# Optimization experiments

Measured on AMD Instinct MI355X. Metric: run time of the kernel, lower is better.

Reference implementation:

```python
import jax, jax.numpy as jnp
import numpy as np

B, T, D = 4, 2048, 1024

def setup_inputs() -> dict:
    key = jax.random.key(0)
    kx, kq, kk, kv = jax.random.split(key, 4)
    lim = 1.0 / np.sqrt(D)
    x = jax.random.normal(kx, (B, T, D), dtype=jnp.float32)
    # nn.Linear weights (stored as [out,in]); applied as x @ W.T
    W_q = jax.random.uniform(kq, (D, D), jnp.float32, -lim, lim)
    W_k = jax.random.uniform(kk, (D, D), jnp.float32, -lim, lim)
    W_v = jax.random.uniform(kv, (D, D), jnp.float32, -lim, lim)
    return {"x": x, "W_q": W_q, "W_k": W_k, "W_v": W_v}

def reference(x, W_q, W_k, W_v):
    d = x.shape[-1]
    Q = jnp.einsum('btd,ed->bte', x, W_q)
    K = jnp.einsum('btd,ed->bte', x, W_k)
    V = jnp.einsum('btd,ed->bte', x, W_v)
    att = jnp.einsum('bqd,bkd->bqk', Q, K) / jnp.sqrt(jnp.asarray(d, x.dtype))
    weights = jax.nn.softmax(att, axis=-1)  # NOTE: original applies no causal mask
    return jnp.einsum('bqk,bkd->bqd', weights, V)
```

## Files before the change

kernel.cpp:

```cpp
#include <hip/hip_runtime.h>
#include <hip/hip_bf16.h>
#include <math.h>
#include <type_traits>


typedef short shortx8 __attribute__((ext_vector_type(8)));
typedef short shortx4 __attribute__((ext_vector_type(4)));
typedef float floatx16 __attribute__((ext_vector_type(16)));
typedef __attribute__((address_space(3))) void lds_void_t;
typedef __attribute__((address_space(1))) const void gmem_void_t;

#define GLD16(gp, lp) \
    __builtin_amdgcn_global_load_lds((gmem_void_t*)(gp), (lds_void_t*)(lp), 16, 0, 0)

#define MODE_PROJ 0
#define MODE_EXP  1
#define MODE_DIV  2

template <int MODE>
__global__ __launch_bounds__(512, 4) void mfma_gemm_abt(
    const __hip_bfloat16* __restrict__ A, const __hip_bfloat16* __restrict__ B,
    void* __restrict__ Cv, float* __restrict__ rowsum,
    __hip_bfloat16* __restrict__ Vt,
    int M, int N, int K, long sA, long sB, long sC, float alpha)
{
    __shared__ __hip_bfloat16 lds[2 * 12288];

    using CT = std::conditional_t<MODE == MODE_DIV, float, __hip_bfloat16>;

    const int z = blockIdx.z;
    A += (long)z * sA;
    B += (long)z * sB;
    CT* C = (CT*)Cv + (long)z * sC;

    const int t     = threadIdx.x;
    const int wave  = t >> 6;
    const int lane  = t & 63;
    const int m0    = blockIdx.x * 256;
    const int n0    = blockIdx.y * 128;
    const int wm    = (wave >> 1) * 64;
    const int wn    = (wave & 1) * 64;
    const int lrow  = lane & 31;
    const int lhalf = lane >> 5;

    const long KU   = (long)(K >> 4);
    const long aOff = (long)((m0 >> 5) + wave) * KU * 512 + lane * 8;
    const long bOff = ((long)((n0 >> 5) + (wave >> 1)) * KU + (wave & 1)) * 512
                      + lane * 8;
    const int  dA   = wave * 1024;
    const int  dB   = 8192 + wave * 512;

    const int raB = (wave >> 1) * 2048 + lane * 8;
    const int rbB = 8192 + (wave & 1) * 2048 + lane * 8;

#define STAGE(bo_, k2_) do {                                               \
        GLD16(A + aOff + (long)(k2_) * 512,       lds + (bo_) + dA);       \
        GLD16(A + aOff + (long)((k2_) + 1) * 512, lds + (bo_) + dA + 512); \
        GLD16(B + bOff + (long)(k2_) * 512,       lds + (bo_) + dB);       \
    } while (0)

    floatx16 acc[2][2] = {};
    const int KT = K >> 5;

    STAGE(0, 0);
    asm volatile("s_waitcnt vmcnt(0)" ::: "memory");
    __builtin_amdgcn_s_barrier();

    for (int kt = 0; kt < KT; ++kt) {
        if (kt + 1 < KT)
            STAGE(((kt + 1) & 1) * 12288, 2 * (kt + 1));

        const __hip_bfloat16* Ls = lds + (kt & 1) * 12288;

        #pragma unroll
        for (int s = 0; s < 2; ++s) {
            shortx8 a[2], b[2];
            #pragma unroll
            for (int i = 0; i < 2; ++i)
                a[i] = *(const shortx8*)(Ls + raB + (2 * i + s) * 512);
            #pragma unroll
            for (int j = 0; j < 2; ++j)
                b[j] = *(const shortx8*)(Ls + rbB + (2 * j + s) * 512);
            __builtin_amdgcn_s_setprio(1);
            #pragma unroll
            for (int i = 0; i < 2; ++i)
                #pragma unroll
                for (int j = 0; j < 2; ++j)
                    acc[i][j] = __builtin_amdgcn_mfma_f32_32x32x16_bf16(
                        a[i], b[j], acc[i][j], 0, 0, 0);
            __builtin_amdgcn_s_setprio(0);
        }
        asm volatile("s_waitcnt vmcnt(0)" ::: "memory");
        __builtin_amdgcn_s_barrier();
    }
#undef STAGE

    auto sidx = [&](int row, int col) -> long {
        return ((long)(row >> 5) * (N >> 4) + (col >> 4)) * 512
             + ((row & 31) + 32 * ((col >> 3) & 1)) * 8 + (col & 7);
    };

    if constexpr (MODE == MODE_PROJ) {
        if (z == 2) {
            const int bz   = m0 >> 11;
            const long bo  = (long)bz * N * 2048;
            #pragma unroll
            for (int i = 0; i < 2; ++i)
                #pragma unroll
                for (int j = 0; j < 2; ++j)
                    #pragma unroll
                    for (int g = 0; g < 4; ++g) {
                        const int t0 = (m0 + wm + 32 * i + g * 8 + 4 * lhalf) & 2047;
                        const int d  = n0 + wn + 32 * j + lrow;
                        shortx4 pk;
                        #pragma unroll
                        for (int r = 0; r < 4; ++r) {
                            __hip_bfloat16 hb = __float2bfloat16(acc[i][j][4 * g + r]);
                            pk[r] = *(short*)&hb;
                        }
                        const long idx = bo
                            + ((long)(d >> 5) * 128 + (t0 >> 4)) * 512
                            + ((d & 31) + 32 * ((t0 >> 3) & 1)) * 8 + (t0 & 7);
                        *(shortx4*)(Vt + idx) = pk;
                    }
        } else {
            #pragma unroll
            for (int i = 0; i < 2; ++i)
                #pragma unroll
                for (int j = 0; j < 2; ++j)
                    #pragma unroll
                    for (int g = 0; g < 4; ++g)
                        #pragma unroll
                        for (int r = 0; r < 4; ++r) {
                            const int row = m0 + wm + 32 * i + g * 8 + 4 * lhalf + r;
                            const int col = n0 + wn + 32 * j + lrow;
                            C[sidx(row, col)] = __float2bfloat16(acc[i][j][4 * g + r]);
                        }
        }
    } else if constexpr (MODE == MODE_EXP) {
        #pragma unroll
        for (int i = 0; i < 2; ++i) {
            float rs[16];
            #pragma unroll
            for (int reg = 0; reg < 16; ++reg) rs[reg] = 0.0f;
            #pragma unroll
            for (int j = 0; j < 2; ++j)
                #pragma unroll
                for (int g = 0; g < 4; ++g)
                    #pragma unroll
                    for (int r = 0; r < 4; ++r) {
                        const int row = m0 + wm + 32 * i + g * 8 + 4 * lhalf + r;
                        const int col = n0 + wn + 32 * j + lrow;
                        const float e = __expf(acc[i][j][4 * g + r] * alpha);
                        rs[4 * g + r] += e;
                        C[sidx(row, col)] = __float2bfloat16(e);
                    }
            #pragma unroll
            for (int reg = 0; reg < 16; ++reg) {
                float v = rs[reg];
                v += __shfl_xor(v, 1);
                v += __shfl_xor(v, 2);
                v += __shfl_xor(v, 4);
                v += __shfl_xor(v, 8);
                v += __shfl_xor(v, 16);
                if (lrow == 0) {
                    const long row = m0 + wm + 32 * i + (reg >> 2) * 8 + 4 * lhalf + (reg & 3);
                    atomicAdd(&rowsum[(long)z * M + row], v);
                }
            }
        }
    } else {
        #pragma unroll
        for (int i = 0; i < 2; ++i) {
            float inv[16];
            #pragma unroll
            for (int g = 0; g < 4; ++g)
                #pragma unroll
                for (int r = 0; r < 4; ++r) {
                    const long row = m0 + wm + 32 * i + g * 8 + 4 * lhalf + r;
                    inv[4 * g + r] = 1.0f / rowsum[(long)z * M + row];
                }
            #pragma unroll
            for (int j = 0; j < 2; ++j)
                #pragma unroll
                for (int g = 0; g < 4; ++g)
                    #pragma unroll
                    for (int r = 0; r < 4; ++r) {
                        const long row = m0 + wm + 32 * i + g * 8 + 4 * lhalf + r;
                        const long col = n0 + wn + 32 * j + lrow;
                        C[row * N + col] = acc[i][j][4 * g + r] * inv[4 * g + r];
                    }
        }
    }
}

__global__ __launch_bounds__(256) void prep(
    const float* __restrict__ x,
    const float* __restrict__ W0, const float* __restrict__ W1,
    const float* __restrict__ W2,
    __hip_bfloat16* __restrict__ xb, __hip_bfloat16* __restrict__ Wb,
    float* __restrict__ rowsum, int n4x, int n4w)
{
    const long i = (long)blockIdx.x * 256 + threadIdx.x;
    if (i < 2048) {
        float4 zz; zz.x = zz.y = zz.z = zz.w = 0.0f;
        ((float4*)rowsum)[i] = zz;
    }
    const float* src;
    __hip_bfloat16* dst;
    long j;
    if (i < n4x) {
        src = x; dst = xb; j = i;
    } else {
        const long k = i - n4x;
        const int w  = (int)(k >> 18);
        j = k & (n4w - 1);
        src = (w == 0) ? W0 : (w == 1) ? W1 : W2;
        dst = Wb + (long)w * n4w * 4;
    }
    const float4 f = ((const float4*)src)[j];
    const int row = (int)(j >> 8);
    const int k0  = (int)(j & 255) * 4;
    const long idx = ((long)(row >> 5) * 64 + (k0 >> 4)) * 512
                   + ((row & 31) + 32 * ((k0 >> 3) & 1)) * 8 + (k0 & 7);
    shortx4 pk;
    __hip_bfloat16 h0 = __float2bfloat16(f.x); pk[0] = *(short*)&h0;
    __hip_bfloat16 h1 = __float2bfloat16(f.y); pk[1] = *(short*)&h1;
    __hip_bfloat16 h2 = __float2bfloat16(f.z); pk[2] = *(short*)&h2;
    __hip_bfloat16 h3 = __float2bfloat16(f.w); pk[3] = *(short*)&h3;
    *(shortx4*)(dst + idx) = pk;
}

extern "C" void kernel_launch(void* const* d_in, const int* in_sizes, int n_in,
                              void* d_out, int out_size, void* d_ws, size_t ws_size,
                              hipStream_t stream)
{
    constexpr int  Bb = 4, T = 2048, D = 1024;
    constexpr int  M  = Bb * T;
    constexpr long TD = (long)T * D;
    constexpr long TT = (long)T * T;
    constexpr long MD = (long)M * D;

    const float* x  = (const float*)d_in[0];
    const float* Wq = (const float*)d_in[1];
    const float* Wk = (const float*)d_in[2];
    const float* Wv = (const float*)d_in[3];
    float* out = (float*)d_out;

    __hip_bfloat16* Q  = (__hip_bfloat16*)d_ws;
    __hip_bfloat16* Kb = Q + MD;
    __hip_bfloat16* Vt = Kb + MD;
    __hip_bfloat16* P  = Vt + MD;
    __hip_bfloat16* xb = P + (long)Bb * TT;
    __hip_bfloat16* Wb = xb + MD;
    float*     rowsum  = (float*)(Wb + 3L * D * D);

    constexpr int n4x = (int)(MD / 4);
    constexpr int n4w = D * D / 4;
    prep<<<dim3((n4x + 3 * n4w) / 256), dim3(256), 0, stream>>>(
        x, Wq, Wk, Wv, xb, Wb, rowsum, n4x, n4w);

    dim3 blk(512);

    mfma_gemm_abt<MODE_PROJ><<<dim3(M / 256, D / 128, 3), blk, 0, stream>>>(
        xb, Wb, Q, nullptr, Vt, M, D, D, 0, (long)D * D, MD, 1.0f);

    mfma_gemm_abt<MODE_EXP><<<dim3(T / 256, T / 128, Bb), blk, 0, stream>>>(
        Q, Kb, P, rowsum, nullptr, T, T, D, TD, TD, TT, 0.03125f);

    mfma_gemm_abt<MODE_DIV><<<dim3(T / 256, D / 128, Bb), blk, 0, stream>>>(
        P, Vt, out, rowsum, nullptr, T, D, T, TT, TD, TD, 1.0f);

    (void)in_sizes; (void)n_in; (void)out_size; (void)ws_size;
}
```

Measured before the change: 257.0 us.

## Triple-buffer GEMM LDS pipeline and stage prep conversion through shared memory

The GEMM main loop goes from double buffering to a three-slot LDS ring. It prefetches two k-tiles ahead and waits only for the oldest batch of loads, so there is one barrier per iteration instead of a full vmcnt(0) drain. The prep kernel now has each block convert a 32-row slab to bf16 into LDS and write it out as contiguous 16-byte stores, replacing scattered 8-byte stores. The cost is 50% more LDS per block (72KB), which may lower occupancy below the four blocks requested in launch bounds, and prep uses far fewer, larger blocks.

Result: faster. 245.6 us (-4.4%).

```diff
diff --git a/kernel.cpp b/kernel.cpp
--- a/kernel.cpp
+++ b/kernel.cpp
@@ -24,7 +24,7 @@
     __hip_bfloat16* __restrict__ Vt,
     int M, int N, int K, long sA, long sB, long sC, float alpha)
 {
-    __shared__ __hip_bfloat16 lds[2 * 12288];
+    __shared__ __hip_bfloat16 lds[3 * 12288];
 
     using CT = std::conditional_t<MODE == MODE_DIV, float, __hip_bfloat16>;
 
@@ -63,14 +63,22 @@
     const int KT = K >> 5;
 
     STAGE(0, 0);
-    asm volatile("s_waitcnt vmcnt(0)" ::: "memory");
-    __builtin_amdgcn_s_barrier();
+    STAGE(12288, 2);
+
+    int rCur = 0;
+    int rNxt = 24576;
 
     for (int kt = 0; kt < KT; ++kt) {
-        if (kt + 1 < KT)
-            STAGE(((kt + 1) & 1) * 12288, 2 * (kt + 1));
-
-        const __hip_bfloat16* Ls = lds + (kt & 1) * 12288;
+        if (kt == KT - 1) {
+            asm volatile("s_waitcnt vmcnt(0)" ::: "memory");
+        } else {
+            asm volatile("s_waitcnt vmcnt(3)" ::: "memory");
+        }
+        __builtin_amdgcn_s_barrier();
+        if (kt + 2 < KT)
+            STAGE(rNxt, 2 * (kt + 2));
+
+        const __hip_bfloat16* Ls = lds + rCur;
 
         #pragma unroll
         for (int s = 0; s < 2; ++s) {
@@ -90,8 +98,8 @@
                         a[i], b[j], acc[i][j], 0, 0, 0);
             __builtin_amdgcn_s_setprio(0);
         }
-        asm volatile("s_waitcnt vmcnt(0)" ::: "memory");
-        __builtin_amdgcn_s_barrier();
+        rCur = (rCur == 24576) ? 0 : rCur + 12288;
+        rNxt = (rNxt == 24576) ? 0 : rNxt + 12288;
     }
 #undef STAGE
 
@@ -199,36 +207,51 @@
     const float* __restrict__ W0, const float* __restrict__ W1,
     const float* __restrict__ W2,
     __hip_bfloat16* __restrict__ xb, __hip_bfloat16* __restrict__ Wb,
-    float* __restrict__ rowsum, int n4x, int n4w)
+    float* __restrict__ rowsum)
 {
-    const long i = (long)blockIdx.x * 256 + threadIdx.x;
-    if (i < 2048) {
+    __shared__ __hip_bfloat16 sb[32768];
+
+    const int b  = blockIdx.x;
+    const int tt = threadIdx.x;
+
+    if (b < 32) {
         float4 zz; zz.x = zz.y = zz.z = zz.w = 0.0f;
-        ((float4*)rowsum)[i] = zz;
-    }
+        ((float4*)rowsum)[b * 256 + tt] = zz;
+    }
+
     const float* src;
     __hip_bfloat16* dst;
-    long j;
-    if (i < n4x) {
-        src = x; dst = xb; j = i;
+    if (b < 256) {
+        src = x + (long)b * 32 * 1024;
+        dst = xb + (long)b * 32768;
     } else {
-        const long k = i - n4x;
-        const int w  = (int)(k >> 18);
-        j = k & (n4w - 1);
-        src = (w == 0) ? W0 : (w == 1) ? W1 : W2;
-        dst = Wb + (long)w * n4w * 4;
-    }
-    const float4 f = ((const float4*)src)[j];
-    const int row = (int)(j >> 8);
-    const int k0  = (int)(j & 255) * 4;
-    const long idx = ((long)(row >> 5) * 64 + (k0 >> 4)) * 512
-                   + ((row & 31) + 32 * ((k0 >> 3) & 1)) * 8 + (k0 & 7);
-    shortx4 pk;
-    __hip_bfloat16 h0 = __float2bfloat16(f.x); pk[0] = *(short*)&h0;
-    __hip_bfloat16 h1 = __float2bfloat16(f.y); pk[1] = *(short*)&h1;
-    __hip_bfloat16 h2 = __float2bfloat16(f.z); pk[2] = *(short*)&h2;
-    __hip_bfloat16 h3 = __float2bfloat16(f.w); pk[3] = *(short*)&h3;
-    *(shortx4*)(dst + idx) = pk;
+        const int w  = (b - 256) >> 5;
+        const int rg = (b - 256) & 31;
+        src = ((w == 0) ? W0 : (w == 1) ? W1 : W2) + (long)rg * 32 * 1024;
+        dst = Wb + (long)w * 1048576 + (long)rg * 32768;
+    }
+
+    #pragma unroll
+    for (int it = 0; it < 32; ++it) {
+        const int idx4 = it * 256 + tt;
+        const float4 f = ((const float4*)src)[idx4];
+        const int row = idx4 >> 8;
+        const int k0  = (idx4 & 255) << 2;
+        const int p   = ((row & 31) + 32 * ((k0 >> 3) & 1)) * 8 + (k0 & 7);
+        shortx4 pk;
+        __hip_bfloat16 h0 = __float2bfloat16(f.x); pk[0] = *(short*)&h0;
+        __hip_bfloat16 h1 = __float2bfloat16(f.y); pk[1] = *(short*)&h1;
+        __hip_bfloat16 h2 = __float2bfloat16(f.z); pk[2] = *(short*)&h2;
+        __hip_bfloat16 h3 = __float2bfloat16(f.w); pk[3] = *(short*)&h3;
+        *(shortx4*)(sb + (k0 >> 4) * 512 + p) = pk;
+    }
+    __syncthreads();
+
+    #pragma unroll
+    for (int ot = 0; ot < 16; ++ot) {
+        const int off = ot * 2048 + tt * 8;
+        *(shortx8*)(dst + off) = *(const shortx8*)(sb + off);
+    }
 }
 
 extern "C" void kernel_launch(void* const* d_in, const int* in_sizes, int n_in,
@@ -255,10 +278,7 @@
     __hip_bfloat16* Wb = xb + MD;
     float*     rowsum  = (float*)(Wb + 3L * D * D);
 
-    constexpr int n4x = (int)(MD / 4);
-    constexpr int n4w = D * D / 4;
-    prep<<<dim3((n4x + 3 * n4w) / 256), dim3(256), 0, stream>>>(
-        x, Wq, Wk, Wv, xb, Wb, rowsum, n4x, n4w);
+    prep<<<dim3(352), dim3(256), 0, stream>>>(x, Wq, Wk, Wv, xb, Wb, rowsum);
 
     dim3 blk(512);
 
```
